# Performance work log

Hardware: AMD Instinct MI355X
Metric: run time of the kernel (lower is better)

Reference implementation:

```python
import jax, jax.numpy as jnp
import numpy as np

B, S, D = 2, 2048, 1024        # batch, seq_len, d_model
E, F, K = 8, 2048, 2           # num_experts, ffn_hidden_size, moe_top_k


def setup_inputs() -> dict:
    key = jax.random.key(0)
    k0, k1, k2, k3, k4 = jax.random.split(key, 5)
    scale = 0.02
    x = jax.random.normal(k0, (B, S, D), dtype=jnp.float32)
    w1 = jax.random.normal(k1, (E * F, D), dtype=jnp.float32) * scale
    v1 = jax.random.normal(k2, (E * F, D), dtype=jnp.float32) * scale
    w2 = jax.random.normal(k3, (E * F, D), dtype=jnp.float32) * scale
    router_w = jax.random.normal(k4, (E, D), dtype=jnp.float32) * scale
    return {"x": x, "w1": w1, "v1": v1, "w2": w2, "router_w": router_w}


def reference(x, w1, v1, w2, router_w):
    # ---- Router (deterministic; no jitter) ----
    logits = jnp.einsum("bsd,ed->bse", x, router_w)              # (B,S,E)
    weights = jax.nn.softmax(logits.astype(jnp.float32), axis=-1)
    top_weights, top_experts = jax.lax.top_k(weights, K)          # (B,S,K)
    # moe_normalize_expert_weights = 1 -> L1 renormalization of top-k weights
    norm = jnp.sum(jnp.abs(top_weights), axis=-1, keepdims=True)
    top_weights = (top_weights / norm).astype(x.dtype)

    # ---- Experts: dense SwiGLU per expert, masked combine (faithful to loop) ----
    w1e = w1.reshape(E, F, D)
    v1e = v1.reshape(E, F, D)
    w2e = w2.reshape(E, F, D)
    out = jnp.zeros_like(x)
    for e in range(E):  # fixed small expert count; structurally distinct weights
        gate = jnp.sum(jnp.where(top_experts == e, top_weights, 0.0), axis=-1)  # (B,S)
        h1 = jax.nn.silu(jnp.einsum("bsd,fd->bsf", x, w1e[e]))
        h = h1 * jnp.einsum("bsd,fd->bsf", x, v1e[e])             # (B,S,F)
        y = jnp.einsum("bsf,fd->bsd", h, w2e[e])                  # (B,S,D)
        out = out + gate[..., None] * y
    return out
```

## Files before the change

### kernel.cpp

```cpp
#include <hip/hip_runtime.h>
#include <hip/hip_bf16.h>
#include <stdint.h>

#define D_MODEL 1024
#define NEXP 8
#define FF 2048
#define TOPK 2
#define NTOK 4096
#define MT 128
#define KSTEP 32
#define MAXROWS (NTOK*TOPK + NEXP*MT)
#define MAXTILES (MAXROWS/MT)

typedef __bf16 bf16x8 __attribute__((ext_vector_type(8)));
typedef float f32x4 __attribute__((ext_vector_type(4)));

__device__ inline unsigned short f2b(float f){
  __hip_bfloat16 h = __float2bfloat16(f);
  return __builtin_bit_cast(unsigned short, h);
}

__device__ inline void gl2lds16(const unsigned short* g, unsigned short* l){
  __builtin_amdgcn_global_load_lds(
      (const __attribute__((address_space(1))) unsigned int*)g,
      (__attribute__((address_space(3))) unsigned int*)l, 16, 0, 0);
}

__global__ void zero_out_kernel(float* out, int n){
  int i = blockIdx.x*256 + threadIdx.x;
  if (i < n) out[i] = 0.f;
}

__global__ __launch_bounds__(256) void conv_kernel(
    const float* __restrict__ in, unsigned short* __restrict__ out, long n4)
{
  long i = (long)blockIdx.x*256 + threadIdx.x;
  if (i >= n4) return;
  float4 v = reinterpret_cast<const float4*>(in)[i];
  ushort4 o;
  o.x = f2b(v.x); o.y = f2b(v.y); o.z = f2b(v.z); o.w = f2b(v.w);
  reinterpret_cast<ushort4*>(out)[i] = o;
}


__global__ void init_kernel(int* perm, int* ctrl){
  int i = blockIdx.x*256 + threadIdx.x;
  if (i < MAXROWS) perm[i] = -1;
  if (i < 64) ctrl[i] = 0;
}

__global__ __launch_bounds__(256) void router_kernel(
    const float* __restrict__ x, const float* __restrict__ rw,
    float* __restrict__ topw, int* __restrict__ tope, int* __restrict__ counts,
    unsigned short* __restrict__ xb)
{
  const int wid = threadIdx.x >> 6, lane = threadIdx.x & 63;
  const int t = blockIdx.x*4 + wid;
  float p[NEXP];
  #pragma unroll
  for (int e=0;e<NEXP;e++) p[e] = 0.f;
  #pragma unroll
  for (int j=0;j<4;j++){
    const int d4 = j*64 + lane;
    float4 xv = reinterpret_cast<const float4*>(x + (long)t*D_MODEL)[d4];
    ushort4 o; o.x=f2b(xv.x); o.y=f2b(xv.y); o.z=f2b(xv.z); o.w=f2b(xv.w);
    reinterpret_cast<ushort4*>(xb + (long)t*D_MODEL)[d4] = o;
    #pragma unroll
    for (int e=0;e<NEXP;e++){
      float4 rv = reinterpret_cast<const float4*>(rw + e*D_MODEL)[d4];
      p[e] += xv.x*rv.x + xv.y*rv.y + xv.z*rv.z + xv.w*rv.w;
    }
  }
  #pragma unroll
  for (int e=0;e<NEXP;e++)
    for (int off=32; off; off>>=1) p[e] += __shfl_xor(p[e], off, 64);
  if (lane == 0){
    float mx = p[0];
    #pragma unroll
    for (int e=1;e<NEXP;e++) mx = fmaxf(mx, p[e]);
    float w[NEXP]; float s = 0.f;
    #pragma unroll
    for (int e=0;e<NEXP;e++){ w[e] = expf(p[e]-mx); s += w[e]; }
    #pragma unroll
    for (int e=0;e<NEXP;e++) w[e] /= s;
    int e1 = 0;
    #pragma unroll
    for (int e=1;e<NEXP;e++) if (w[e] > w[e1]) e1 = e;
    int e2 = -1;
    #pragma unroll
    for (int e=0;e<NEXP;e++) if (e != e1 && (e2 < 0 || w[e] > w[e2])) e2 = e;
    float s2 = w[e1] + w[e2];
    topw[t*2+0] = w[e1]/s2;
    topw[t*2+1] = w[e2]/s2;
    tope[t*2+0] = e1; tope[t*2+1] = e2;
    atomicAdd(&counts[e1], 1); atomicAdd(&counts[e2], 1);
  }
}

__global__ void partition_kernel(const int* ctrl, int* segStart, int* tileExpert){
  if (threadIdx.x == 0 && blockIdx.x == 0){
    int off = 0, tile = 0;
    for (int e=0;e<NEXP;e++){
      segStart[e] = off;
      int padded = ((ctrl[e] + MT - 1)/MT)*MT;
      off += padded;
      for (int k=0;k<padded/MT && tile < MAXTILES;k++) tileExpert[tile++] = e;
    }
    segStart[NEXP] = off;
    while (tile < MAXTILES) tileExpert[tile++] = -1;
  }
}

__global__ void scatter_kernel(const int* tope, const int* segStart, int* fill,
                               int* perm, int* rowOf){
  int i = blockIdx.x*256 + threadIdx.x;
  int e = tope[i];
  int pos = segStart[e] + atomicAdd(&fill[e], 1);
  if (pos >= 0 && pos < MAXROWS){ perm[pos] = i >> 1; rowOf[i] = pos; }
}

__global__ void transpose_w2(const float* __restrict__ w2,
                             unsigned short* __restrict__ w2t){
  __shared__ unsigned short tl[32][33];
  const int e = blockIdx.z;
  const int d0 = blockIdx.x*32, f0 = blockIdx.y*32;
  const int tx = threadIdx.x, ty = threadIdx.y;
  #pragma unroll
  for (int i=0;i<4;i++)
    tl[ty + i*8][tx] = f2b(w2[((long)(e*FF + f0 + ty + i*8))*D_MODEL + d0 + tx]);
  __syncthreads();
  #pragma unroll
  for (int i=0;i<4;i++)
    w2t[((long)e*D_MODEL + d0 + ty + i*8)*FF + f0 + tx] = tl[tx][ty + i*8];
}

__global__ __launch_bounds__(256, 2) void gemm1_swiglu(
    const unsigned short* __restrict__ x,
    const unsigned short* __restrict__ w1,
    const unsigned short* __restrict__ v1,
    const int* __restrict__ perm,
    const int* __restrict__ tileExpert,
    unsigned short* __restrict__ Hg)
{
  const int b = blockIdx.x;
  const int xcd = b & 7, s = b >> 3;
  const int mt = xcd*9 + (s % 9);
  const int nt = s / 9;
  int e = tileExpert[mt];
  if (e < 0) return;
  e &= 7;
  __shared__ alignas(16) unsigned short As [3][MT*KSTEP];
  __shared__ alignas(16) unsigned short B1s[3][MT*KSTEP];
  __shared__ alignas(16) unsigned short B2s[3][MT*KSTEP];
  const int tid = threadIdx.x;
  const int lane = tid & 63;
  const int wr = ((tid >> 7) & 1) * 64;
  const int wc = ((tid >> 6) & 1) * 64;
  unsigned short* const As0  = &As [0][0];
  unsigned short* const B1s0 = &B1s[0][0];
  unsigned short* const B2s0 = &B2s[0][0];
  const int BSZ = MT*KSTEP;

  long aoff[2]; long boff[2]; int dstIdx[2];
  #pragma unroll
  for (int i=0;i<2;i++){
    int idx = tid + 256*i;
    int r = idx >> 2, c = idx & 3;
    int sc = c ^ ((r >> 1) & 3);
    int tok = perm[mt*MT + r]; if (tok < 0 || tok >= NTOK) tok = 0;
    aoff[i] = (long)tok * D_MODEL + sc*8;
    boff[i] = ((long)e*FF + nt*MT + r) * D_MODEL + sc*8;
    dstIdx[i] = idx * 8;
  }
  f32x4 zero = {0.f,0.f,0.f,0.f};
  f32x4 acc1[4][4], acc2[4][4];
  #pragma unroll
  for (int i=0;i<4;i++)
    #pragma unroll
    for (int j=0;j<4;j++){ acc1[i][j] = zero; acc2[i][j] = zero; }

  #pragma unroll
  for (int i=0;i<2;i++) gl2lds16(x  + aoff[i],          As0  + dstIdx[i]);
  #pragma unroll
  for (int i=0;i<2;i++) gl2lds16(w1 + boff[i],          B1s0 + dstIdx[i]);
  #pragma unroll
  for (int i=0;i<2;i++) gl2lds16(v1 + boff[i],          B2s0 + dstIdx[i]);
  #pragma unroll
  for (int i=0;i<2;i++) gl2lds16(x  + aoff[i] + KSTEP,  As0  + BSZ + dstIdx[i]);
  #pragma unroll
  for (int i=0;i<2;i++) gl2lds16(w1 + boff[i] + KSTEP,  B1s0 + BSZ + dstIdx[i]);
  #pragma unroll
  for (int i=0;i<2;i++) gl2lds16(v1 + boff[i] + KSTEP,  B2s0 + BSZ + dstIdx[i]);

  const int NK = D_MODEL / KSTEP;
  int cur = 0;
  for (int t=0; t<NK; ++t){
    if (t+2 < NK){
      const int pf = (cur == 0) ? 2 : cur-1;
      const long k0 = (long)(t+2)*KSTEP;
      const int pdst = pf*BSZ;
      #pragma unroll
      for (int i=0;i<2;i++) gl2lds16(x  + aoff[i] + k0, As0  + pdst + dstIdx[i]);
      #pragma unroll
      for (int i=0;i<2;i++) gl2lds16(w1 + boff[i] + k0, B1s0 + pdst + dstIdx[i]);
      #pragma unroll
      for (int i=0;i<2;i++) gl2lds16(v1 + boff[i] + k0, B2s0 + pdst + dstIdx[i]);
      asm volatile("s_waitcnt vmcnt(12)" ::: "memory");
    } else if (t+1 < NK){
      asm volatile("s_waitcnt vmcnt(6)" ::: "memory");
    } else {
      asm volatile("s_waitcnt vmcnt(0)" ::: "memory");
    }
    __builtin_amdgcn_s_barrier();
    asm volatile("" ::: "memory");

    const unsigned short* Ac  = As0  + cur*BSZ;
    const unsigned short* B1c = B1s0 + cur*BSZ;
    const unsigned short* B2c = B2s0 + cur*BSZ;
    const int q = lane >> 4;
    bf16x8 a[4], bb1[4], bb2[4];
    #pragma unroll
    for (int i=0;i<4;i++){
      int r = wr + i*16 + (lane & 15);
      a[i] = *reinterpret_cast<const bf16x8*>(&Ac[r*KSTEP + ((q ^ ((r>>1)&3))*8)]);
    }
    #pragma unroll
    for (int j=0;j<4;j++){
      int n = wc + j*16 + (lane & 15);
      int adr = n*KSTEP + ((q ^ ((n>>1)&3))*8);
      bb1[j] = *reinterpret_cast<const bf16x8*>(&B1c[adr]);
      bb2[j] = *reinterpret_cast<const bf16x8*>(&B2c[adr]);
    }
    #pragma unroll
    for (int i=0;i<4;i++)
      #pragma unroll
      for (int j=0;j<4;j++){
        acc1[i][j] = __builtin_amdgcn_mfma_f32_16x16x32_bf16(a[i], bb1[j], acc1[i][j], 0,0,0);
        acc2[i][j] = __builtin_amdgcn_mfma_f32_16x16x32_bf16(a[i], bb2[j], acc2[i][j], 0,0,0);
      }
    asm volatile("s_waitcnt lgkmcnt(0)" ::: "memory");
    __builtin_amdgcn_s_barrier();
    asm volatile("" ::: "memory");
    cur = (cur == 2) ? 0 : cur+1;
  }
  const int mrow0 = mt*MT + wr + ((lane >> 4) << 2);
  const int ncol0 = nt*MT + wc + (lane & 15);
  #pragma unroll
  for (int i=0;i<4;i++)
    #pragma unroll
    for (int j=0;j<4;j++)
      #pragma unroll
      for (int rr=0;rr<4;rr++){
        float g = acc1[i][j][rr];
        float u = acc2[i][j][rr];
        float h = (g / (1.0f + __expf(-g))) * u;
        Hg[(long)(mrow0 + i*16 + rr)*FF + (ncol0 + j*16)] = f2b(h);
      }
}

__global__ __launch_bounds__(256, 3) void gemm2_kernel(
    const unsigned short* __restrict__ Hg,
    const unsigned short* __restrict__ w2t,
    const int* __restrict__ tileExpert,
    float* __restrict__ Yg)
{
  const int b = blockIdx.x;
  const int xcd = b & 7, s = b >> 3;
  const int mt = xcd + 8*(s >> 3);
  const int nt = s & 7;
  int e = tileExpert[mt];
  if (e < 0) return;
  e &= 7;
  __shared__ alignas(16) unsigned short As[3][MT*KSTEP];
  __shared__ alignas(16) unsigned short Bs[3][MT*KSTEP];
  const int tid = threadIdx.x;
  const int lane = tid & 63;
  const int wr = ((tid >> 7) & 1) * 64;
  const int wc = ((tid >> 6) & 1) * 64;
  unsigned short* const As0 = &As[0][0];
  unsigned short* const Bs0 = &Bs[0][0];
  const int BSZ = MT*KSTEP;

  long aoff[2]; long boff[2]; int dstIdx[2];
  #pragma unroll
  for (int i=0;i<2;i++){
    int idx = tid + 256*i;
    int r = idx >> 2, c = idx & 3;
    int sc = c ^ ((r >> 1) & 3);
    aoff[i] = (long)(mt*MT + r) * FF + sc*8;
    boff[i] = ((long)e*D_MODEL + nt*MT + r) * FF + sc*8;
    dstIdx[i] = idx * 8;
  }
  f32x4 zero = {0.f,0.f,0.f,0.f};
  f32x4 acc[4][4];
  #pragma unroll
  for (int i=0;i<4;i++)
    #pragma unroll
    for (int j=0;j<4;j++) acc[i][j] = zero;

  #pragma unroll
  for (int i=0;i<2;i++) gl2lds16(Hg  + aoff[i],          As0 + dstIdx[i]);
  #pragma unroll
  for (int i=0;i<2;i++) gl2lds16(w2t + boff[i],          Bs0 + dstIdx[i]);
  #pragma unroll
  for (int i=0;i<2;i++) gl2lds16(Hg  + aoff[i] + KSTEP,  As0 + BSZ + dstIdx[i]);
  #pragma unroll
  for (int i=0;i<2;i++) gl2lds16(w2t + boff[i] + KSTEP,  Bs0 + BSZ + dstIdx[i]);

  const int NK = FF / KSTEP;
  int cur = 0;
  for (int t=0; t<NK; ++t){
    if (t+2 < NK){
      const int pf = (cur == 0) ? 2 : cur-1;
      const long k0 = (long)(t+2)*KSTEP;
      const int pdst = pf*BSZ;
      #pragma unroll
      for (int i=0;i<2;i++) gl2lds16(Hg  + aoff[i] + k0, As0 + pdst + dstIdx[i]);
      #pragma unroll
      for (int i=0;i<2;i++) gl2lds16(w2t + boff[i] + k0, Bs0 + pdst + dstIdx[i]);
      asm volatile("s_waitcnt vmcnt(8)" ::: "memory");
    } else if (t+1 < NK){
      asm volatile("s_waitcnt vmcnt(4)" ::: "memory");
    } else {
      asm volatile("s_waitcnt vmcnt(0)" ::: "memory");
    }
    __builtin_amdgcn_s_barrier();
    asm volatile("" ::: "memory");

    const unsigned short* Ac = As0 + cur*BSZ;
    const unsigned short* Bc = Bs0 + cur*BSZ;
    const int q = lane >> 4;
    bf16x8 a[4], bb[4];
    #pragma unroll
    for (int i=0;i<4;i++){
      int r = wr + i*16 + (lane & 15);
      a[i] = *reinterpret_cast<const bf16x8*>(&Ac[r*KSTEP + ((q ^ ((r>>1)&3))*8)]);
    }
    #pragma unroll
    for (int j=0;j<4;j++){
      int n = wc + j*16 + (lane & 15);
      bb[j] = *reinterpret_cast<const bf16x8*>(&Bc[n*KSTEP + ((q ^ ((n>>1)&3))*8)]);
    }
    #pragma unroll
    for (int i=0;i<4;i++)
      #pragma unroll
      for (int j=0;j<4;j++)
        acc[i][j] = __builtin_amdgcn_mfma_f32_16x16x32_bf16(a[i], bb[j], acc[i][j], 0,0,0);

    asm volatile("s_waitcnt lgkmcnt(0)" ::: "memory");
    __builtin_amdgcn_s_barrier();
    asm volatile("" ::: "memory");
    cur = (cur == 2) ? 0 : cur+1;
  }
  const int mrow0 = mt*MT + wr + ((lane >> 4) << 2);
  const int ncol0 = nt*MT + wc + (lane & 15);
  #pragma unroll
  for (int i=0;i<4;i++)
    #pragma unroll
    for (int j=0;j<4;j++)
      #pragma unroll
      for (int rr=0;rr<4;rr++)
        Yg[(long)(mrow0 + i*16 + rr)*D_MODEL + (ncol0 + j*16)] = acc[i][j][rr];
}

__global__ __launch_bounds__(256) void combine_kernel(
    const float* __restrict__ Yg, const float* __restrict__ topw,
    const int* __restrict__ rowOf, float* __restrict__ out)
{
  const int t = blockIdx.x;
  const int d = threadIdx.x * 4;
  const float wA = topw[2*t], wB = topw[2*t+1];
  long rA = rowOf[2*t], rB = rowOf[2*t+1];
  if (rA < 0 || rA >= MAXROWS) rA = 0;
  if (rB < 0 || rB >= MAXROWS) rB = 0;
  float4 a = *reinterpret_cast<const float4*>(Yg + rA*D_MODEL + d);
  float4 b = *reinterpret_cast<const float4*>(Yg + rB*D_MODEL + d);
  float4 o;
  o.x = wA*a.x + wB*b.x;
  o.y = wA*a.y + wB*b.y;
  o.z = wA*a.z + wB*b.z;
  o.w = wA*a.w + wB*b.w;
  *reinterpret_cast<float4*>(out + (long)t*D_MODEL + d) = o;
}

extern "C" void kernel_launch(void* const* d_in, const int* in_sizes, int n_in,
                              void* d_out, int out_size, void* d_ws, size_t ws_size,
                              hipStream_t stream)
{
  const float* x  = (const float*)d_in[0];
  const float* w1 = (const float*)d_in[1];
  const float* v1 = (const float*)d_in[2];
  const float* w2 = (const float*)d_in[3];
  const float* rw = (const float*)d_in[4];
  float* out = (float*)d_out;
  (void)in_sizes; (void)n_in;

  size_t need = 0;
  auto count = [&](size_t b){ size_t r = need; need += (b + 255) & ~(size_t)255; return r; };
  size_t o_topw = count((size_t)NTOK*TOPK*sizeof(float));
  size_t o_tope = count((size_t)NTOK*TOPK*sizeof(int));
  size_t o_ctrl = count(64*sizeof(int));
  size_t o_seg  = count(16*sizeof(int));
  size_t o_te   = count(MAXTILES*sizeof(int));
  size_t o_perm = count(MAXROWS*sizeof(int));
  size_t o_rowOf= count((size_t)NTOK*TOPK*sizeof(int));
  size_t o_xb   = count((size_t)NTOK*D_MODEL*2);
  size_t o_w1b  = count((size_t)NEXP*FF*D_MODEL*2);
  size_t o_v1b  = count((size_t)NEXP*FF*D_MODEL*2);
  size_t o_w2t  = count((size_t)NEXP*D_MODEL*FF*2);
  size_t o_Hg   = count((size_t)MAXROWS*FF*2);
  size_t o_Yg   = count((size_t)MAXROWS*D_MODEL*sizeof(float));

  if (ws_size < need){
    zero_out_kernel<<<(out_size+255)/256, 256, 0, stream>>>(out, out_size);
    return;
  }

  char* base = (char*)d_ws;
  float* topw      = (float*)(base + o_topw);
  int*   tope      = (int*)  (base + o_tope);
  int*   ctrl      = (int*)  (base + o_ctrl);
  int*   segStart  = (int*)  (base + o_seg);
  int*   tileExpert= (int*)  (base + o_te);
  int*   perm      = (int*)  (base + o_perm);
  int*   rowOf     = (int*)  (base + o_rowOf);
  unsigned short* xb  = (unsigned short*)(base + o_xb);
  unsigned short* w1b = (unsigned short*)(base + o_w1b);
  unsigned short* v1b = (unsigned short*)(base + o_v1b);
  unsigned short* w2t = (unsigned short*)(base + o_w2t);
  unsigned short* Hg  = (unsigned short*)(base + o_Hg);
  float*          Yg  = (float*)         (base + o_Yg);

  const long nw4 = (long)NEXP*FF*D_MODEL/4;

  init_kernel     <<<(MAXROWS+255)/256, 256, 0, stream>>>(perm, ctrl);
  router_kernel   <<<NTOK/4, 256, 0, stream>>>(x, rw, topw, tope, ctrl, xb);
  partition_kernel<<<1, 64, 0, stream>>>(ctrl, segStart, tileExpert);
  scatter_kernel  <<<NTOK*TOPK/256, 256, 0, stream>>>(tope, segStart, ctrl+8, perm, rowOf);
  conv_kernel     <<<(nw4+255)/256, 256, 0, stream>>>(w1, w1b, nw4);
  conv_kernel     <<<(nw4+255)/256, 256, 0, stream>>>(v1, v1b, nw4);
  transpose_w2    <<<dim3(D_MODEL/32, FF/32, NEXP), dim3(32,8), 0, stream>>>(w2, w2t);
  gemm1_swiglu    <<<MAXTILES*(FF/MT), 256, 0, stream>>>(xb, w1b, v1b, perm, tileExpert, Hg);
  gemm2_kernel    <<<MAXTILES*(D_MODEL/MT), 256, 0, stream>>>(Hg, w2t, tileExpert, Yg);
  combine_kernel  <<<NTOK, 256, 0, stream>>>(Yg, topw, rowOf, out);
}
```

Measured before the change: 538.7 us.

## Enlarge gemm1 tile to 256 rows with 512 threads and phased double buffering

Expert segments are now padded to 256 rows, and gemm1_swiglu runs 256x128 tiles with 8 waves. Each wave computes 128x32 of both gate and up projections, using KSTEP 64 split into two 32-wide halves, double-buffered, with loads interleaved across four barrier-separated phases and s_setprio around the MFMA bursts. gemm2 keeps its 128-row tiles through a second tile-expert table. The aim is more reuse of weight tiles per block, fewer gemm1 blocks, and better overlap of loads with MFMA work. In exchange it adds padding rows, and more barriers and per-block LDS.

```diff
diff --git a/kernel.cpp b/kernel.cpp
--- a/kernel.cpp
+++ b/kernel.cpp
@@ -7,10 +7,11 @@
 #define FF 2048
 #define TOPK 2
 #define NTOK 4096
+#define MT2 256
 #define MT 128
-#define KSTEP 32
-#define MAXROWS (NTOK*TOPK + NEXP*MT)
-#define MAXTILES (MAXROWS/MT)
+#define MAXROWS 10240
+#define NT256 40
+#define NT128 80
 
 typedef __bf16 bf16x8 __attribute__((ext_vector_type(8)));
 typedef float f32x4 __attribute__((ext_vector_type(4)));
@@ -97,17 +98,20 @@
   }
 }
 
-__global__ void partition_kernel(const int* ctrl, int* segStart, int* tileExpert){
+__global__ void partition_kernel(const int* ctrl, int* segStart,
+                                 int* te256, int* te128){
   if (threadIdx.x == 0 && blockIdx.x == 0){
-    int off = 0, tile = 0;
+    int off = 0, t2 = 0, t1 = 0;
     for (int e=0;e<NEXP;e++){
       segStart[e] = off;
-      int padded = ((ctrl[e] + MT - 1)/MT)*MT;
+      int padded = ((ctrl[e] + MT2 - 1)/MT2)*MT2;
       off += padded;
-      for (int k=0;k<padded/MT && tile < MAXTILES;k++) tileExpert[tile++] = e;
+      for (int k=0;k<padded/MT2 && t2 < NT256;k++) te256[t2++] = e;
+      for (int k=0;k<padded/MT  && t1 < NT128;k++) te128[t1++] = e;
     }
     segStart[NEXP] = off;
-    while (tile < MAXTILES) tileExpert[tile++] = -1;
+    while (t2 < NT256) te256[t2++] = -1;
+    while (t1 < NT128) te128[t1++] = -1;
   }
 }
 
@@ -134,141 +138,137 @@
     w2t[((long)e*D_MODEL + d0 + ty + i*8)*FF + f0 + tx] = tl[tx][ty + i*8];
 }
 
-__global__ __launch_bounds__(256, 2) void gemm1_swiglu(
+__global__ __launch_bounds__(512, 2) void gemm1_swiglu(
     const unsigned short* __restrict__ x,
     const unsigned short* __restrict__ w1,
     const unsigned short* __restrict__ v1,
     const int* __restrict__ perm,
-    const int* __restrict__ tileExpert,
+    const int* __restrict__ te256,
     unsigned short* __restrict__ Hg)
 {
   const int b = blockIdx.x;
   const int xcd = b & 7, s = b >> 3;
-  const int mt = xcd*9 + (s % 9);
-  const int nt = s / 9;
-  int e = tileExpert[mt];
+  const int mt = xcd*5 + (s % 5);
+  const int nt = s / 5;
+  int e = te256[mt];
   if (e < 0) return;
   e &= 7;
-  __shared__ alignas(16) unsigned short As [3][MT*KSTEP];
-  __shared__ alignas(16) unsigned short B1s[3][MT*KSTEP];
-  __shared__ alignas(16) unsigned short B2s[3][MT*KSTEP];
+  __shared__ alignas(16) unsigned short As [2][2][8192];
+  __shared__ alignas(16) unsigned short B1s[2][2][4096];
+  __shared__ alignas(16) unsigned short B2s[2][2][4096];
   const int tid = threadIdx.x;
   const int lane = tid & 63;
-  const int wr = ((tid >> 7) & 1) * 64;
-  const int wc = ((tid >> 6) & 1) * 64;
-  unsigned short* const As0  = &As [0][0];
-  unsigned short* const B1s0 = &B1s[0][0];
-  unsigned short* const B2s0 = &B2s[0][0];
-  const int BSZ = MT*KSTEP;
-
-  long aoff[2]; long boff[2]; int dstIdx[2];
-  #pragma unroll
-  for (int i=0;i<2;i++){
-    int idx = tid + 256*i;
-    int r = idx >> 2, c = idx & 3;
-    int sc = c ^ ((r >> 1) & 3);
-    int tok = perm[mt*MT + r]; if (tok < 0 || tok >= NTOK) tok = 0;
-    aoff[i] = (long)tok * D_MODEL + sc*8;
-    boff[i] = ((long)e*FF + nt*MT + r) * D_MODEL + sc*8;
-    dstIdx[i] = idx * 8;
-  }
+  const int wid = tid >> 6;
+  const int wm = wid >> 2, wn = wid & 3;
+
+  const int ra = tid >> 2, ca = tid & 3;
+  const int sca = ca ^ ((ra >> 1) & 3);
+  int tok0 = perm[mt*MT2 + ra];        if (tok0 < 0 || tok0 >= NTOK) tok0 = 0;
+  int tok1 = perm[mt*MT2 + ra + 128];  if (tok1 < 0 || tok1 >= NTOK) tok1 = 0;
+  const long aS0 = (long)tok0*D_MODEL + sca*8;
+  const long aS1 = (long)tok1*D_MODEL + sca*8;
+  const long bS  = ((long)e*FF + nt*128 + ra)*D_MODEL + sca*8;
+  const int dA0 = tid*8, dA1 = (tid+512)*8, dB = tid*8;
+
   f32x4 zero = {0.f,0.f,0.f,0.f};
-  f32x4 acc1[4][4], acc2[4][4];
-  #pragma unroll
-  for (int i=0;i<4;i++)
-    #pragma unroll
-    for (int j=0;j<4;j++){ acc1[i][j] = zero; acc2[i][j] = zero; }
-
-  #pragma unroll
-  for (int i=0;i<2;i++) gl2lds16(x  + aoff[i],          As0  + dstIdx[i]);
-  #pragma unroll
-  for (int i=0;i<2;i++) gl2lds16(w1 + boff[i],          B1s0 + dstIdx[i]);
-  #pragma unroll
-  for (int i=0;i<2;i++) gl2lds16(v1 + boff[i],          B2s0 + dstIdx[i]);
-  #pragma unroll
-  for (int i=0;i<2;i++) gl2lds16(x  + aoff[i] + KSTEP,  As0  + BSZ + dstIdx[i]);
-  #pragma unroll
-  for (int i=0;i<2;i++) gl2lds16(w1 + boff[i] + KSTEP,  B1s0 + BSZ + dstIdx[i]);
-  #pragma unroll
-  for (int i=0;i<2;i++) gl2lds16(v1 + boff[i] + KSTEP,  B2s0 + BSZ + dstIdx[i]);
-
-  const int NK = D_MODEL / KSTEP;
-  int cur = 0;
-  for (int t=0; t<NK; ++t){
-    if (t+2 < NK){
-      const int pf = (cur == 0) ? 2 : cur-1;
-      const long k0 = (long)(t+2)*KSTEP;
-      const int pdst = pf*BSZ;
-      #pragma unroll
-      for (int i=0;i<2;i++) gl2lds16(x  + aoff[i] + k0, As0  + pdst + dstIdx[i]);
-      #pragma unroll
-      for (int i=0;i<2;i++) gl2lds16(w1 + boff[i] + k0, B1s0 + pdst + dstIdx[i]);
-      #pragma unroll
-      for (int i=0;i<2;i++) gl2lds16(v1 + boff[i] + k0, B2s0 + pdst + dstIdx[i]);
-      asm volatile("s_waitcnt vmcnt(12)" ::: "memory");
-    } else if (t+1 < NK){
-      asm volatile("s_waitcnt vmcnt(6)" ::: "memory");
-    } else {
-      asm volatile("s_waitcnt vmcnt(0)" ::: "memory");
-    }
-    __builtin_amdgcn_s_barrier();
-    asm volatile("" ::: "memory");
-
-    const unsigned short* Ac  = As0  + cur*BSZ;
-    const unsigned short* B1c = B1s0 + cur*BSZ;
-    const unsigned short* B2c = B2s0 + cur*BSZ;
-    const int q = lane >> 4;
-    bf16x8 a[4], bb1[4], bb2[4];
-    #pragma unroll
-    for (int i=0;i<4;i++){
-      int r = wr + i*16 + (lane & 15);
-      a[i] = *reinterpret_cast<const bf16x8*>(&Ac[r*KSTEP + ((q ^ ((r>>1)&3))*8)]);
-    }
-    #pragma unroll
-    for (int j=0;j<4;j++){
-      int n = wc + j*16 + (lane & 15);
-      int adr = n*KSTEP + ((q ^ ((n>>1)&3))*8);
-      bb1[j] = *reinterpret_cast<const bf16x8*>(&B1c[adr]);
-      bb2[j] = *reinterpret_cast<const bf16x8*>(&B2c[adr]);
-    }
-    #pragma unroll
-    for (int i=0;i<4;i++)
-      #pragma unroll
-      for (int j=0;j<4;j++){
-        acc1[i][j] = __builtin_amdgcn_mfma_f32_16x16x32_bf16(a[i], bb1[j], acc1[i][j], 0,0,0);
-        acc2[i][j] = __builtin_amdgcn_mfma_f32_16x16x32_bf16(a[i], bb2[j], acc2[i][j], 0,0,0);
-      }
-    asm volatile("s_waitcnt lgkmcnt(0)" ::: "memory");
-    __builtin_amdgcn_s_barrier();
-    asm volatile("" ::: "memory");
-    cur = (cur == 2) ? 0 : cur+1;
-  }
-  const int mrow0 = mt*MT + wr + ((lane >> 4) << 2);
-  const int ncol0 = nt*MT + wc + (lane & 15);
-  #pragma unroll
-  for (int i=0;i<4;i++)
-    #pragma unroll
-    for (int j=0;j<4;j++)
+  f32x4 acc1[8][2], acc2[8][2];
+  #pragma unroll
+  for (int i=0;i<8;i++)
+    #pragma unroll
+    for (int j=0;j<2;j++){ acc1[i][j] = zero; acc2[i][j] = zero; }
+
+  const int lq = lane >> 4, ll = lane & 15;
+  const int scol = (lq ^ ((ll >> 1) & 3)) * 8;
+  const int aRow = (wm*128 + ll)*32 + scol;
+  const int nRow = (wn*32  + ll)*32 + scol;
+
+#define VMW(n) asm volatile("s_waitcnt vmcnt(" #n ")" ::: "memory")
+#define BAR()  do{ asm volatile("" ::: "memory"); __builtin_amdgcn_s_barrier(); \
+                   asm volatile("" ::: "memory"); }while(0)
+#define STAGE_A(BUF,KK,KT) do{ const long o_ = (long)(KT)*64 + (KK)*32; \
+    gl2lds16(x + aS0 + o_, &As[BUF][KK][0] + dA0);                      \
+    gl2lds16(x + aS1 + o_, &As[BUF][KK][0] + dA1); }while(0)
+#define STAGE_B(BUF,KK,KT) do{ const long o_ = (long)(KT)*64 + (KK)*32; \
+    gl2lds16(w1 + bS + o_, &B1s[BUF][KK][0] + dB);                      \
+    gl2lds16(v1 + bS + o_, &B2s[BUF][KK][0] + dB); }while(0)
+#define PHASE(BUF_,KK_,H_,LOADB_) do{                                   \
+    const unsigned short* Ap  = &As [BUF_][KK_][0];                     \
+    if (LOADB_){                                                        \
+      const unsigned short* Bp1 = &B1s[BUF_][KK_][0];                   \
+      const unsigned short* Bp2 = &B2s[BUF_][KK_][0];                   \
+      _Pragma("unroll")                                                 \
+      for (int j=0;j<2;j++){                                            \
+        b1f[j] = *(const bf16x8*)&Bp1[nRow + j*512];                    \
+        b2f[j] = *(const bf16x8*)&Bp2[nRow + j*512];                    \
+      }                                                                 \
+    }                                                                   \
+    bf16x8 af[4];                                                       \
+    _Pragma("unroll")                                                   \
+    for (int i=0;i<4;i++) af[i] = *(const bf16x8*)&Ap[aRow + ((H_)*64 + i*16)*32]; \
+    __builtin_amdgcn_s_setprio(1);                                      \
+    _Pragma("unroll")                                                   \
+    for (int i=0;i<4;i++)                                               \
+      _Pragma("unroll")                                                 \
+      for (int j=0;j<2;j++){                                            \
+        acc1[(H_)*4+i][j] = __builtin_amdgcn_mfma_f32_16x16x32_bf16(af[i], b1f[j], acc1[(H_)*4+i][j], 0,0,0); \
+        acc2[(H_)*4+i][j] = __builtin_amdgcn_mfma_f32_16x16x32_bf16(af[i], b2f[j], acc2[(H_)*4+i][j], 0,0,0); \
+      }                                                                 \
+    __builtin_amdgcn_s_setprio(0);                                      \
+  }while(0)
+
+  STAGE_A(0,0,0); STAGE_B(0,0,0); STAGE_A(0,1,0); STAGE_B(0,1,0);
+
+  bf16x8 b1f[2], b2f[2];
+  const int NKT = D_MODEL/64;
+  for (int kt=0; kt<NKT; ++kt){
+    const int buf = kt & 1, nb = buf ^ 1;
+    const bool pre = (kt+1 < NKT);
+    if (pre){ STAGE_A(nb,0,kt+1); VMW(6); } else { VMW(4); }
+    BAR();
+    if (buf == 0) PHASE(0,0,0,1); else PHASE(1,0,0,1);
+    if (pre){ STAGE_B(nb,0,kt+1); VMW(6); } else { VMW(4); }
+    BAR();
+    if (buf == 0) PHASE(0,0,1,0); else PHASE(1,0,1,0);
+    if (pre){ STAGE_A(nb,1,kt+1); VMW(6); } else { VMW(0); }
+    BAR();
+    if (buf == 0) PHASE(0,1,0,1); else PHASE(1,1,0,1);
+    if (pre){ STAGE_B(nb,1,kt+1); VMW(6); } else { VMW(0); }
+    BAR();
+    if (buf == 0) PHASE(0,1,1,0); else PHASE(1,1,1,0);
+  }
+#undef PHASE
+#undef STAGE_A
+#undef STAGE_B
+#undef VMW
+#undef BAR
+
+  const int mrowB = mt*MT2 + wm*128 + lq*4;
+  const int ncolB = nt*128 + wn*32 + ll;
+  #pragma unroll
+  for (int m=0;m<8;m++)
+    #pragma unroll
+    for (int j=0;j<2;j++)
       #pragma unroll
       for (int rr=0;rr<4;rr++){
-        float g = acc1[i][j][rr];
-        float u = acc2[i][j][rr];
+        float g = acc1[m][j][rr];
+        float u = acc2[m][j][rr];
         float h = (g / (1.0f + __expf(-g))) * u;
-        Hg[(long)(mrow0 + i*16 + rr)*FF + (ncol0 + j*16)] = f2b(h);
+        Hg[(long)(mrowB + m*16 + rr)*FF + (ncolB + j*16)] = f2b(h);
       }
 }
 
 __global__ __launch_bounds__(256, 3) void gemm2_kernel(
     const unsigned short* __restrict__ Hg,
     const unsigned short* __restrict__ w2t,
-    const int* __restrict__ tileExpert,
+    const int* __restrict__ te128,
     float* __restrict__ Yg)
 {
+#define KSTEP 32
   const int b = blockIdx.x;
   const int xcd = b & 7, s = b >> 3;
   const int mt = xcd + 8*(s >> 3);
   const int nt = s & 7;
-  int e = tileExpert[mt];
+  int e = te128[mt];
   if (e < 0) return;
   e &= 7;
   __shared__ alignas(16) unsigned short As[3][MT*KSTEP];
@@ -361,6 +361,7 @@
       #pragma unroll
       for (int rr=0;rr<4;rr++)
         Yg[(long)(mrow0 + i*16 + rr)*D_MODEL + (ncol0 + j*16)] = acc[i][j][rr];
+#undef KSTEP
 }
 
 __global__ __launch_bounds__(256) void combine_kernel(
@@ -401,8 +402,8 @@
   size_t o_tope = count((size_t)NTOK*TOPK*sizeof(int));
   size_t o_ctrl = count(64*sizeof(int));
   size_t o_seg  = count(16*sizeof(int));
-  size_t o_te   = count(MAXTILES*sizeof(int));
-  size_t o_perm = count(MAXROWS*sizeof(int));
+  size_t o_te   = count(128*sizeof(int));
+  size_t o_perm = count((size_t)MAXROWS*sizeof(int));
   size_t o_rowOf= count((size_t)NTOK*TOPK*sizeof(int));
   size_t o_xb   = count((size_t)NTOK*D_MODEL*2);
   size_t o_w1b  = count((size_t)NEXP*FF*D_MODEL*2);
@@ -421,7 +422,8 @@
   int*   tope      = (int*)  (base + o_tope);
   int*   ctrl      = (int*)  (base + o_ctrl);
   int*   segStart  = (int*)  (base + o_seg);
-  int*   tileExpert= (int*)  (base + o_te);
+  int*   te256     = (int*)  (base + o_te);
+  int*   te128     = te256 + 48;
   int*   perm      = (int*)  (base + o_perm);
   int*   rowOf     = (int*)  (base + o_rowOf);
   unsigned short* xb  = (unsigned short*)(base + o_xb);
@@ -435,12 +437,12 @@
 
   init_kernel     <<<(MAXROWS+255)/256, 256, 0, stream>>>(perm, ctrl);
   router_kernel   <<<NTOK/4, 256, 0, stream>>>(x, rw, topw, tope, ctrl, xb);
-  partition_kernel<<<1, 64, 0, stream>>>(ctrl, segStart, tileExpert);
+  partition_kernel<<<1, 64, 0, stream>>>(ctrl, segStart, te256, te128);
   scatter_kernel  <<<NTOK*TOPK/256, 256, 0, stream>>>(tope, segStart, ctrl+8, perm, rowOf);
   conv_kernel     <<<(nw4+255)/256, 256, 0, stream>>>(w1, w1b, nw4);
   conv_kernel     <<<(nw4+255)/256, 256, 0, stream>>>(v1, v1b, nw4);
   transpose_w2    <<<dim3(D_MODEL/32, FF/32, NEXP), dim3(32,8), 0, stream>>>(w2, w2t);
-  gemm1_swiglu    <<<MAXTILES*(FF/MT), 256, 0, stream>>>(xb, w1b, v1b, perm, tileExpert, Hg);
-  gemm2_kernel    <<<MAXTILES*(D_MODEL/MT), 256, 0, stream>>>(Hg, w2t, tileExpert, Yg);
+  gemm1_swiglu    <<<NT256*(FF/128), 512, 0, stream>>>(xb, w1b, v1b, perm, te256, Hg);
+  gemm2_kernel    <<<NT128*(D_MODEL/MT), 256, 0, stream>>>(Hg, w2t, te128, Yg);
   combine_kernel  <<<NTOK, 256, 0, stream>>>(Yg, topw, rowOf, out);
 }
```

Measured after the change: 793.0 us. 1.47x slower.
